# Kernel optimization log

Measured on AMD Instinct MI355X. Metric: run time of the kernel, lower is better.

## Reference

```python
import jax, jax.numpy as jnp
import numpy as np

N = 50000   # nodes
E = 1600000 # edges (avg degree 32)
IN, D, OUT = 128, 256, 128
NUM_MID = 8  # num_layers - 2


def gcn_conv(x, W, b, src, dst, n):
    """PyG GCNConv: add self-loops, symmetric norm, linear transform, scatter-sum."""
    h = x @ W                                           # [n, d_out]
    ones = jnp.ones(src.shape[0], h.dtype)
    deg = jax.ops.segment_sum(ones, dst, num_segments=n) + 1.0  # +1 self-loop
    dinv = jax.lax.rsqrt(deg)                           # deg^{-1/2}
    coef = dinv[src] * dinv[dst]                        # [E]
    agg = jax.ops.segment_sum(h[src] * coef[:, None], dst, num_segments=n)
    agg = agg + h * (dinv * dinv)[:, None]              # self-loop term: dinv[i]^2
    return agg + b


def layer_norm(x, g, b, eps=1e-5):
    mu = jnp.mean(x, axis=-1, keepdims=True)
    var = jnp.mean(jnp.square(x - mu), axis=-1, keepdims=True)
    return (x - mu) * jax.lax.rsqrt(var + eps) * g + b


def setup_inputs() -> dict:
    key = jax.random.key(0)
    ks = jax.random.split(key, 8)
    x = jax.random.normal(ks[0], (N, IN), dtype=jnp.float32)
    edge_index = jax.random.randint(ks[1], (2, E), 0, N, dtype=jnp.int64)
    s_in = 1.0 / np.sqrt(IN)
    s_d = 1.0 / np.sqrt(D)
    return {
        "x": x,
        "edge_index": edge_index,
        "W_in": jax.random.normal(ks[2], (IN, D), dtype=jnp.float32) * s_in,
        "b_in": jnp.zeros((D,), jnp.float32),
        "W_mid": jax.random.normal(ks[3], (NUM_MID, D, D), dtype=jnp.float32) * s_d,
        "b_mid": jnp.zeros((NUM_MID, D), jnp.float32),
        "W_out": jax.random.normal(ks[4], (D, OUT), dtype=jnp.float32) * s_d,
        "b_out": jnp.zeros((OUT,), jnp.float32),
        "gamma": jnp.ones((NUM_MID + 1, D), jnp.float32),
        "beta": jnp.zeros((NUM_MID + 1, D), jnp.float32),
    }


def reference(x, edge_index, W_in, b_in, W_mid, b_mid, W_out, b_out, gamma, beta):
    # Inference mode: dropout is identity.
    src, dst = edge_index[0], edge_index[1]
    n = x.shape[0]
    h = gcn_conv(x, W_in, b_in, src, dst, n)
    h = jax.nn.silu(layer_norm(h, gamma[0], beta[0]))
    for i in range(NUM_MID):  # fixed small layer count
        h = gcn_conv(h, W_mid[i], b_mid[i], src, dst, n)
        h = jax.nn.silu(layer_norm(h, gamma[i + 1], beta[i + 1]))
    return gcn_conv(h, W_out, b_out, src, dst, n)
```

## Files before the change

kernel.cpp:

```cpp
#include <hip/hip_runtime.h>
#include <stdint.h>

#define NN   50000
#define NE   1600000
#define DIN  128
#define DMID 256
#define DOUT 128
#define NMID 8

#define AS1 __attribute__((address_space(1)))
#define AS3 __attribute__((address_space(3)))

typedef unsigned short u16;
typedef unsigned int   u32;
typedef __attribute__((ext_vector_type(8))) short short8;
typedef __attribute__((ext_vector_type(4))) float f32x4;
typedef __attribute__((ext_vector_type(2))) float f32x2;
typedef __attribute__((ext_vector_type(4))) int i32x4;

__device__ __forceinline__ float bf2f(u32 u) {
    union { u32 i; float f; } c; c.i = u << 16; return c.f;
}
__device__ __forceinline__ u16 f2bf(float f) {
    union { float f; u32 i; } c; c.f = f;
    u32 u = c.i;
    return (u16)((u + 0x7fffu + ((u >> 16) & 1u)) >> 16);
}
__device__ __forceinline__ void split2(float v, u16& hi, u16& lo) {
    hi = f2bf(v);
    float r = v - bf2f(hi);
    lo = f2bf(r);
}

__global__ void rank_kernel(const int* __restrict__ ei, int* __restrict__ counts,
                            int* __restrict__ rank) {
    int i = (blockIdx.x * blockDim.x + threadIdx.x) * 4;
    if (i < NE) {
        i32x4 d = *(const i32x4*)(ei + NE + i);
        i32x4 r;
        r.x = atomicAdd(&counts[d.x], 1);
        r.y = atomicAdd(&counts[d.y], 1);
        r.z = atomicAdd(&counts[d.z], 1);
        r.w = atomicAdd(&counts[d.w], 1);
        *(i32x4*)(rank + i) = r;
    }
}

__global__ void dinv_kernel(const int* __restrict__ counts, float* __restrict__ dinv) {
    int i = blockIdx.x * blockDim.x + threadIdx.x;
    if (i < NN) dinv[i] = rsqrtf((float)counts[i] + 1.0f);
}

__global__ __launch_bounds__(1024) void scan_kernel(const int* __restrict__ counts,
                                                    int* __restrict__ rowp) {
    __shared__ int sh[1024];
    const int t = threadIdx.x;
    constexpr int ITEMS = (NN + 1023) / 1024;
    const int start = t * ITEMS;
    int sum = 0;
    for (int j = 0; j < ITEMS; ++j) {
        int idx = start + j;
        if (idx < NN) sum += counts[idx];
    }
    sh[t] = sum;
    __syncthreads();
    for (int offs = 1; offs < 1024; offs <<= 1) {
        int v = (t >= offs) ? sh[t - offs] : 0;
        __syncthreads();
        sh[t] += v;
        __syncthreads();
    }
    int base = (t == 0) ? 0 : sh[t - 1];
    for (int j = 0; j < ITEMS; ++j) {
        int idx = start + j;
        if (idx < NN) {
            rowp[idx] = base;
            base += counts[idx];
        }
    }
    if (t == 0) rowp[NN] = NE;
}

__global__ void scatter_kernel(const int* __restrict__ ei, const int* __restrict__ rowp,
                               const int* __restrict__ rank, int* __restrict__ srcs) {
    int i = (blockIdx.x * blockDim.x + threadIdx.x) * 4;
    if (i < NE) {
        i32x4 d = *(const i32x4*)(ei + NE + i);
        i32x4 s = *(const i32x4*)(ei + i);
        i32x4 r = *(const i32x4*)(rank + i);
        srcs[rowp[d.x] + r.x] = s.x;
        srcs[rowp[d.y] + r.y] = s.y;
        srcs[rowp[d.z] + r.z] = s.z;
        srcs[rowp[d.w] + r.w] = s.w;
    }
}

__global__ void wsplit_kernel(const float* __restrict__ W, u16* __restrict__ Whi,
                              u16* __restrict__ Wlo, int K, int Dc) {
    int idx = blockIdx.x * blockDim.x + threadIdx.x;
    if (idx < K * Dc) {
        int k = idx / Dc, d = idx - k * Dc;
        u16 hi, lo;
        split2(W[idx], hi, lo);
        size_t o = ((size_t)(k >> 5) * Dc + d) * 32 + (k & 31);
        Whi[o] = hi;
        Wlo[o] = lo;
    }
}

__global__ void xsplit_kernel(const float* __restrict__ x, u16* __restrict__ xhi,
                              u16* __restrict__ xlo) {
    int i = blockIdx.x * blockDim.x + threadIdx.x;
    int stride = gridDim.x * blockDim.x;
    for (; i < NN * DIN; i += stride) {
        u16 hi, lo;
        split2(x[i], hi, lo);
        xhi[i] = hi;
        xlo[i] = lo;
    }
}


template <int K, int Dc>
__global__ __launch_bounds__(512, 4) void gemm_kernel(const u16* __restrict__ xhi,
                                                      const u16* __restrict__ xlo,
                                                      const u16* __restrict__ whi,
                                                      const u16* __restrict__ wlo,
                                                      const float* __restrict__ dinv,
                                                      u16* __restrict__ g) {
    constexpr int NTW = Dc / 32;
    constexpr int KS = K / 32;
    __shared__ u16 bh[Dc * 32];
    __shared__ u16 bl[Dc * 32];
    const int tid = threadIdx.x;
    const int wid = tid >> 6;
    const int rowPanel = wid >> 1;
    const int colPanel = wid & 1;
    const int lane = tid & 63;
    const int m = lane & 15, quad = lane >> 4;
    const int rowBase = blockIdx.x * 128 + rowPanel * 32;

    f32x4 acc[2][NTW];
#pragma unroll
    for (int rg = 0; rg < 2; ++rg)
#pragma unroll
        for (int t = 0; t < NTW; ++t) acc[rg][t] = (f32x4){0.f, 0.f, 0.f, 0.f};

    size_t arow[2];
#pragma unroll
    for (int rg = 0; rg < 2; ++rg) {
        int rowA = rowBase + rg * 16 + m;
        if (rowA > NN - 1) rowA = NN - 1;
        arow[rg] = (size_t)rowA * K + quad * 8;
    }

    for (int ks = 0; ks < KS; ++ks) {
        const u16* sh_src = whi + (size_t)ks * Dc * 32;
        const u16* sl_src = wlo + (size_t)ks * Dc * 32;
        __syncthreads();
#pragma unroll
        for (int i = 0; i < Dc * 4; i += 512) {
            int j = i + tid;
            __builtin_amdgcn_global_load_lds((const AS1 void*)(sh_src + j * 8),
                                             (AS3 void*)((AS3 u16*)bh + j * 8), 16, 0, 0);
            __builtin_amdgcn_global_load_lds((const AS1 void*)(sl_src + j * 8),
                                             (AS3 void*)((AS3 u16*)bl + j * 8), 16, 0, 0);
        }
        short8 ah[2], al[2];
#pragma unroll
        for (int rg = 0; rg < 2; ++rg) {
            ah[rg] = *(const short8*)(xhi + arow[rg] + ks * 32);
            al[rg] = *(const short8*)(xlo + arow[rg] + ks * 32);
        }
        __syncthreads();
#pragma unroll
        for (int t = 0; t < NTW; ++t) {
            const int bo = ((colPanel * NTW + t) * 16 + m) * 32 + quad * 8;
            short8 wh = *(const short8*)(bh + bo);
            short8 wl = *(const short8*)(bl + bo);
#pragma unroll
            for (int rg = 0; rg < 2; ++rg) {
                acc[rg][t] = __builtin_amdgcn_mfma_f32_16x16x32_bf16(ah[rg], wh, acc[rg][t], 0, 0, 0);
                acc[rg][t] = __builtin_amdgcn_mfma_f32_16x16x32_bf16(al[rg], wh, acc[rg][t], 0, 0, 0);
                acc[rg][t] = __builtin_amdgcn_mfma_f32_16x16x32_bf16(ah[rg], wl, acc[rg][t], 0, 0, 0);
            }
        }
    }

#pragma unroll
    for (int rg = 0; rg < 2; ++rg) {
        const int r0 = rowBase + rg * 16 + quad * 4;
        float dv[4];
#pragma unroll
        for (int r = 0; r < 4; ++r) {
            int rr = r0 + r;
            dv[r] = (rr < NN) ? dinv[rr] : 0.f;
        }
#pragma unroll
        for (int t = 0; t < NTW; ++t) {
            const int col = colPanel * (Dc / 2) + t * 16 + m;
#pragma unroll
            for (int r = 0; r < 4; ++r) {
                int rr = r0 + r;
                if (rr < NN) g[(size_t)rr * Dc + col] = f2bf(acc[rg][t][r] * dv[r]);
            }
        }
    }
}


template <int L>
__device__ __forceinline__ void loadg(const u16* p, float (&f)[L]);
template <>
__device__ __forceinline__ void loadg<4>(const u16* p, float (&f)[4]) {
    uint2 v = *(const uint2*)p;
    f[0] = bf2f(v.x & 0xffffu); f[1] = bf2f(v.x >> 16);
    f[2] = bf2f(v.y & 0xffffu); f[3] = bf2f(v.y >> 16);
}
template <>
__device__ __forceinline__ void loadg<2>(const u16* p, float (&f)[2]) {
    u32 v = *(const u32*)p;
    f[0] = bf2f(v & 0xffffu); f[1] = bf2f(v >> 16);
}

template <int Dc, bool FINAL>
__global__ __launch_bounds__(256) void agg_kernel(const u16* __restrict__ g,
                                                  const int* __restrict__ rowp,
                                                  const int* __restrict__ srcs,
                                                  const float* __restrict__ dinv,
                                                  const float* __restrict__ bias,
                                                  const float* __restrict__ gamma,
                                                  const float* __restrict__ beta,
                                                  float* __restrict__ outf,
                                                  u16* __restrict__ xhi,
                                                  u16* __restrict__ xlo) {
    constexpr int L = Dc / 64;
    const int wid = threadIdx.x >> 6, lane = threadIdx.x & 63;
    const int node = blockIdx.x * 4 + wid;
    const int coff = lane * L;

    float acc[L];
    loadg<L>(g + (size_t)node * Dc + coff, acc);

    int e = rowp[node];
    const int end = rowp[node + 1];
    for (; e + 8 <= end; e += 8) {
        int s0 = srcs[e],     s1 = srcs[e + 1], s2 = srcs[e + 2], s3 = srcs[e + 3];
        int s4 = srcs[e + 4], s5 = srcs[e + 5], s6 = srcs[e + 6], s7 = srcs[e + 7];
        float f0[L], f1[L], f2[L], f3[L], f4[L], f5[L], f6[L], f7[L];
        loadg<L>(g + (size_t)s0 * Dc + coff, f0);
        loadg<L>(g + (size_t)s1 * Dc + coff, f1);
        loadg<L>(g + (size_t)s2 * Dc + coff, f2);
        loadg<L>(g + (size_t)s3 * Dc + coff, f3);
        loadg<L>(g + (size_t)s4 * Dc + coff, f4);
        loadg<L>(g + (size_t)s5 * Dc + coff, f5);
        loadg<L>(g + (size_t)s6 * Dc + coff, f6);
        loadg<L>(g + (size_t)s7 * Dc + coff, f7);
#pragma unroll
        for (int j = 0; j < L; ++j)
            acc[j] += ((f0[j] + f1[j]) + (f2[j] + f3[j])) +
                      ((f4[j] + f5[j]) + (f6[j] + f7[j]));
    }
    for (; e < end; ++e) {
        float f[L];
        loadg<L>(g + (size_t)srcs[e] * Dc + coff, f);
#pragma unroll
        for (int j = 0; j < L; ++j) acc[j] += f[j];
    }

    const float dv = dinv[node];
    float v[L];
#pragma unroll
    for (int j = 0; j < L; ++j) v[j] = acc[j] * dv + bias[coff + j];

    if (FINAL) {
        if (L == 4) {
            f32x4 o = {v[0], v[1], v[2], v[3]};
            *(f32x4*)(outf + (size_t)node * Dc + coff) = o;
        } else {
            f32x2 o = {v[0], v[1]};
            *(f32x2*)(outf + (size_t)node * Dc + coff) = o;
        }
    } else {
        float s = 0.f, s2 = 0.f;
#pragma unroll
        for (int j = 0; j < L; ++j) {
            s += v[j];
            s2 += v[j] * v[j];
        }
        for (int off = 32; off > 0; off >>= 1) {
            s += __shfl_xor(s, off, 64);
            s2 += __shfl_xor(s2, off, 64);
        }
        const float mu = s * (1.f / Dc);
        const float var = s2 * (1.f / Dc) - mu * mu;
        const float rstd = rsqrtf(fmaxf(var, 0.f) + 1e-5f);
#pragma unroll
        for (int j = 0; j < L; ++j) {
            float y = (v[j] - mu) * rstd * gamma[coff + j] + beta[coff + j];
            v[j] = y / (1.f + __expf(-y));
        }
        u16 hh[L], ll[L];
#pragma unroll
        for (int j = 0; j < L; ++j) split2(v[j], hh[j], ll[j]);
        if (L == 4) {
            uint2 oh, ol;
            oh.x = (u32)hh[0] | ((u32)hh[1] << 16);
            oh.y = (u32)hh[2] | ((u32)hh[3] << 16);
            ol.x = (u32)ll[0] | ((u32)ll[1] << 16);
            ol.y = (u32)ll[2] | ((u32)ll[3] << 16);
            *(uint2*)(xhi + (size_t)node * Dc + coff) = oh;
            *(uint2*)(xlo + (size_t)node * Dc + coff) = ol;
        } else {
            *(u32*)(xhi + (size_t)node * Dc + coff) = (u32)hh[0] | ((u32)hh[1] << 16);
            *(u32*)(xlo + (size_t)node * Dc + coff) = (u32)ll[0] | ((u32)ll[1] << 16);
        }
    }
}


extern "C" void kernel_launch(void* const* d_in, const int* in_sizes, int n_in,
                              void* d_out, int out_size, void* d_ws, size_t ws_size,
                              hipStream_t stream) {
    (void)in_sizes; (void)n_in; (void)out_size; (void)ws_size;
    const float* x_in  = (const float*)d_in[0];
    const int*   ei    = (const int*)d_in[1];
    const float* W_in  = (const float*)d_in[2];
    const float* b_in  = (const float*)d_in[3];
    const float* W_mid = (const float*)d_in[4];
    const float* b_mid = (const float*)d_in[5];
    const float* W_out = (const float*)d_in[6];
    const float* b_out = (const float*)d_in[7];
    const float* gamma = (const float*)d_in[8];
    const float* beta  = (const float*)d_in[9];

    char* ws = (char*)d_ws;
    size_t off = 0;
    auto alloc = [&](size_t bytes) -> char* {
        char* p = ws + off;
        off += (bytes + 255) & ~(size_t)255;
        return p;
    };
    float* dinv   = (float*)alloc((size_t)NN * 4);
    int* counts   = (int*)alloc((size_t)NN * 4);
    int* rowp     = (int*)alloc((size_t)(NN + 1) * 4);
    int* rank     = (int*)alloc((size_t)NE * 4);
    int* srcs     = (int*)alloc((size_t)NE * 4);
    u16* whi_in   = (u16*)alloc((size_t)DIN * DMID * 2);
    u16* wlo_in   = (u16*)alloc((size_t)DIN * DMID * 2);
    u16* whi_mid  = (u16*)alloc((size_t)NMID * DMID * DMID * 2);
    u16* wlo_mid  = (u16*)alloc((size_t)NMID * DMID * DMID * 2);
    u16* whi_out  = (u16*)alloc((size_t)DMID * DOUT * 2);
    u16* wlo_out  = (u16*)alloc((size_t)DMID * DOUT * 2);
    u16* xhi      = (u16*)alloc((size_t)NN * DMID * 2);
    u16* xlo      = (u16*)alloc((size_t)NN * DMID * 2);
    u16* g        = (u16*)alloc((size_t)NN * DMID * 2);

    hipMemsetAsync(counts, 0, (size_t)NN * 4, stream);
    const int EB4 = (NE / 4 + 255) / 256;
    rank_kernel<<<EB4, 256, 0, stream>>>(ei, counts, rank);
    dinv_kernel<<<(NN + 255) / 256, 256, 0, stream>>>(counts, dinv);
    scan_kernel<<<1, 1024, 0, stream>>>(counts, rowp);
    scatter_kernel<<<EB4, 256, 0, stream>>>(ei, rowp, rank, srcs);

    wsplit_kernel<<<(DIN * DMID + 255) / 256, 256, 0, stream>>>(W_in, whi_in, wlo_in, DIN, DMID);
    for (int i = 0; i < NMID; ++i)
        wsplit_kernel<<<(DMID * DMID + 255) / 256, 256, 0, stream>>>(
            W_mid + (size_t)i * DMID * DMID, whi_mid + (size_t)i * DMID * DMID,
            wlo_mid + (size_t)i * DMID * DMID, DMID, DMID);
    wsplit_kernel<<<(DMID * DOUT + 255) / 256, 256, 0, stream>>>(W_out, whi_out, wlo_out, DMID, DOUT);
    xsplit_kernel<<<1024, 256, 0, stream>>>(x_in, xhi, xlo);

    const int GB = (NN + 127) / 128;
    const int NB = NN / 4;

    gemm_kernel<DIN, DMID><<<GB, 512, 0, stream>>>(xhi, xlo, whi_in, wlo_in, dinv, g);
    agg_kernel<DMID, false><<<NB, 256, 0, stream>>>(g, rowp, srcs, dinv, b_in,
                                                    gamma, beta, nullptr, xhi, xlo);
    for (int i = 0; i < NMID; ++i) {
        gemm_kernel<DMID, DMID><<<GB, 512, 0, stream>>>(xhi, xlo,
                                                        whi_mid + (size_t)i * DMID * DMID,
                                                        wlo_mid + (size_t)i * DMID * DMID,
                                                        dinv, g);
        agg_kernel<DMID, false><<<NB, 256, 0, stream>>>(g, rowp, srcs, dinv,
                                                        b_mid + (size_t)i * DMID,
                                                        gamma + (size_t)(i + 1) * DMID,
                                                        beta + (size_t)(i + 1) * DMID,
                                                        nullptr, xhi, xlo);
    }
    gemm_kernel<DMID, DOUT><<<GB, 512, 0, stream>>>(xhi, xlo, whi_out, wlo_out, dinv, g);
    agg_kernel<DOUT, true><<<NB, 256, 0, stream>>>(g, rowp, srcs, dinv, b_out,
                                                   nullptr, nullptr, (float*)d_out,
                                                   nullptr, nullptr);
}
```

Baseline: 1.647 ms.

## Bucket CSR neighbors by source chunk, pad rows, and software-pipeline gathers

The CSR build now groups each node's incoming edges by source-id chunk (source >> 11), so gathers from g walk memory in a more local order. Each row is padded to a multiple of 8 with a dummy index that points at a zeroed extra row of g, which removes the tail loop. The aggregation loop is double-buffered so the next eight row gathers are issued before the current eight are summed, and blocks now hold 8 warps instead of 4. In exchange, preprocessing needs extra kernels and buffers (counts2, rowp2, padded srcs), and the padding adds wasted gather work.

```diff
diff --git a/kernel.cpp b/kernel.cpp
--- a/kernel.cpp
+++ b/kernel.cpp
@@ -7,6 +7,9 @@
 #define DMID 256
 #define DOUT 128
 #define NMID 8
+#define CSH  11
+#define CH   25
+#define PADCAP (NE + 7 * NN)
 
 #define AS1 __attribute__((address_space(1)))
 #define AS3 __attribute__((address_space(3)))
@@ -21,6 +24,12 @@
 __device__ __forceinline__ float bf2f(u32 u) {
     union { u32 i; float f; } c; c.i = u << 16; return c.f;
 }
+__device__ __forceinline__ float ubf_lo(u32 v) {
+    union { u32 i; float f; } c; c.i = v << 16; return c.f;
+}
+__device__ __forceinline__ float ubf_hi(u32 v) {
+    union { u32 i; float f; } c; c.i = v & 0xffff0000u; return c.f;
+}
 __device__ __forceinline__ u16 f2bf(float f) {
     union { float f; u32 i; } c; c.f = f;
     u32 u = c.i;
@@ -32,23 +41,30 @@
     lo = f2bf(r);
 }
 
-__global__ void rank_kernel(const int* __restrict__ ei, int* __restrict__ counts,
+__global__ void rank_kernel(const int* __restrict__ ei, int* __restrict__ counts2,
                             int* __restrict__ rank) {
     int i = (blockIdx.x * blockDim.x + threadIdx.x) * 4;
     if (i < NE) {
         i32x4 d = *(const i32x4*)(ei + NE + i);
+        i32x4 s = *(const i32x4*)(ei + i);
         i32x4 r;
-        r.x = atomicAdd(&counts[d.x], 1);
-        r.y = atomicAdd(&counts[d.y], 1);
-        r.z = atomicAdd(&counts[d.z], 1);
-        r.w = atomicAdd(&counts[d.w], 1);
+        r.x = atomicAdd(&counts2[d.x * CH + (s.x >> CSH)], 1);
+        r.y = atomicAdd(&counts2[d.y * CH + (s.y >> CSH)], 1);
+        r.z = atomicAdd(&counts2[d.z * CH + (s.z >> CSH)], 1);
+        r.w = atomicAdd(&counts2[d.w * CH + (s.w >> CSH)], 1);
         *(i32x4*)(rank + i) = r;
     }
 }
 
-__global__ void dinv_kernel(const int* __restrict__ counts, float* __restrict__ dinv) {
+__global__ void sumc_kernel(const int* __restrict__ counts2, int* __restrict__ counts,
+                            float* __restrict__ dinv) {
     int i = blockIdx.x * blockDim.x + threadIdx.x;
-    if (i < NN) dinv[i] = rsqrtf((float)counts[i] + 1.0f);
+    if (i < NN) {
+        int s = 0;
+        for (int c = 0; c < CH; ++c) s += counts2[i * CH + c];
+        dinv[i] = rsqrtf((float)s + 1.0f);
+        counts[i] = (s + 7) & ~7;
+    }
 }
 
 __global__ __launch_bounds__(1024) void scan_kernel(const int* __restrict__ counts,
@@ -76,22 +92,39 @@
         if (idx < NN) {
             rowp[idx] = base;
             base += counts[idx];
-        }
-    }
-    if (t == 0) rowp[NN] = NE;
-}
-
-__global__ void scatter_kernel(const int* __restrict__ ei, const int* __restrict__ rowp,
+            if (idx == NN - 1) rowp[NN] = base;
+        }
+    }
+}
+
+__global__ void rowp2_kernel(const int* __restrict__ counts2, const int* __restrict__ rowp,
+                             int* __restrict__ rowp2) {
+    int i = blockIdx.x * blockDim.x + threadIdx.x;
+    if (i < NN) {
+        int base = rowp[i];
+        for (int c = 0; c < CH; ++c) {
+            rowp2[i * CH + c] = base;
+            base += counts2[i * CH + c];
+        }
+    }
+}
+
+__global__ void fill_kernel(int* __restrict__ srcs) {
+    int i = (blockIdx.x * blockDim.x + threadIdx.x) * 4;
+    if (i < PADCAP) *(i32x4*)(srcs + i) = (i32x4){NN, NN, NN, NN};
+}
+
+__global__ void scatter_kernel(const int* __restrict__ ei, const int* __restrict__ rowp2,
                                const int* __restrict__ rank, int* __restrict__ srcs) {
     int i = (blockIdx.x * blockDim.x + threadIdx.x) * 4;
     if (i < NE) {
         i32x4 d = *(const i32x4*)(ei + NE + i);
         i32x4 s = *(const i32x4*)(ei + i);
         i32x4 r = *(const i32x4*)(rank + i);
-        srcs[rowp[d.x] + r.x] = s.x;
-        srcs[rowp[d.y] + r.y] = s.y;
-        srcs[rowp[d.z] + r.z] = s.z;
-        srcs[rowp[d.w] + r.w] = s.w;
+        srcs[rowp2[d.x * CH + (s.x >> CSH)] + r.x] = s.x;
+        srcs[rowp2[d.y * CH + (s.y >> CSH)] + r.y] = s.y;
+        srcs[rowp2[d.z * CH + (s.z >> CSH)] + r.z] = s.z;
+        srcs[rowp2[d.w * CH + (s.w >> CSH)] + r.w] = s.w;
     }
 }
 
@@ -119,7 +152,6 @@
         xlo[i] = lo;
     }
 }
-
 
 template <int K, int Dc>
 __global__ __launch_bounds__(512, 4) void gemm_kernel(const u16* __restrict__ xhi,
@@ -214,17 +246,47 @@
 template <>
 __device__ __forceinline__ void loadg<4>(const u16* p, float (&f)[4]) {
     uint2 v = *(const uint2*)p;
-    f[0] = bf2f(v.x & 0xffffu); f[1] = bf2f(v.x >> 16);
-    f[2] = bf2f(v.y & 0xffffu); f[3] = bf2f(v.y >> 16);
+    f[0] = ubf_lo(v.x); f[1] = ubf_hi(v.x);
+    f[2] = ubf_lo(v.y); f[3] = ubf_hi(v.y);
 }
 template <>
 __device__ __forceinline__ void loadg<2>(const u16* p, float (&f)[2]) {
     u32 v = *(const u32*)p;
-    f[0] = bf2f(v & 0xffffu); f[1] = bf2f(v >> 16);
+    f[0] = ubf_lo(v); f[1] = ubf_hi(v);
+}
+
+__device__ __forceinline__ void load_srcs(const int* __restrict__ srcs, int eo,
+                                          int (&S)[8]) {
+#pragma unroll
+    for (int k = 0; k < 8; ++k) S[k] = srcs[eo + k];
+}
+
+template <int Dc, int L>
+__device__ __forceinline__ void issue_rows(const u16* __restrict__ g, const int (&S)[8],
+                                           int coff, uint2 (&R)[8]) {
+#pragma unroll
+    for (int k = 0; k < 8; ++k) {
+        const u16* p = g + (size_t)S[k] * Dc + coff;
+        if constexpr (L == 4) R[k] = *(const uint2*)p;
+        else R[k].x = *(const u32*)p;
+    }
+}
+
+template <int L>
+__device__ __forceinline__ void consume(const uint2 (&R)[8], float (&acc)[L]) {
+#pragma unroll
+    for (int k = 0; k < 8; ++k) {
+        acc[0] += ubf_lo(R[k].x);
+        acc[1] += ubf_hi(R[k].x);
+        if constexpr (L == 4) {
+            acc[2] += ubf_lo(R[k].y);
+            acc[3] += ubf_hi(R[k].y);
+        }
+    }
 }
 
 template <int Dc, bool FINAL>
-__global__ __launch_bounds__(256) void agg_kernel(const u16* __restrict__ g,
+__global__ __launch_bounds__(512) void agg_kernel(const u16* __restrict__ g,
                                                   const int* __restrict__ rowp,
                                                   const int* __restrict__ srcs,
                                                   const float* __restrict__ dinv,
@@ -236,36 +298,38 @@
                                                   u16* __restrict__ xlo) {
     constexpr int L = Dc / 64;
     const int wid = threadIdx.x >> 6, lane = threadIdx.x & 63;
-    const int node = blockIdx.x * 4 + wid;
+    const int node = blockIdx.x * 8 + wid;
     const int coff = lane * L;
 
     float acc[L];
     loadg<L>(g + (size_t)node * Dc + coff, acc);
 
-    int e = rowp[node];
-    const int end = rowp[node + 1];
-    for (; e + 8 <= end; e += 8) {
-        int s0 = srcs[e],     s1 = srcs[e + 1], s2 = srcs[e + 2], s3 = srcs[e + 3];
-        int s4 = srcs[e + 4], s5 = srcs[e + 5], s6 = srcs[e + 6], s7 = srcs[e + 7];
-        float f0[L], f1[L], f2[L], f3[L], f4[L], f5[L], f6[L], f7[L];
-        loadg<L>(g + (size_t)s0 * Dc + coff, f0);
-        loadg<L>(g + (size_t)s1 * Dc + coff, f1);
-        loadg<L>(g + (size_t)s2 * Dc + coff, f2);
-        loadg<L>(g + (size_t)s3 * Dc + coff, f3);
-        loadg<L>(g + (size_t)s4 * Dc + coff, f4);
-        loadg<L>(g + (size_t)s5 * Dc + coff, f5);
-        loadg<L>(g + (size_t)s6 * Dc + coff, f6);
-        loadg<L>(g + (size_t)s7 * Dc + coff, f7);
-#pragma unroll
-        for (int j = 0; j < L; ++j)
-            acc[j] += ((f0[j] + f1[j]) + (f2[j] + f3[j])) +
-                      ((f4[j] + f5[j]) + (f6[j] + f7[j]));
-    }
-    for (; e < end; ++e) {
-        float f[L];
-        loadg<L>(g + (size_t)srcs[e] * Dc + coff, f);
-#pragma unroll
-        for (int j = 0; j < L; ++j) acc[j] += f[j];
+    const int e0 = rowp[node];
+    const int nb = (rowp[node + 1] - e0) >> 3;
+
+    if (nb > 0) {
+        const int last = e0 + (nb - 1) * 8;
+        int S[8];
+        uint2 rA[8], rB[8];
+        load_srcs(srcs, e0, S);
+        issue_rows<Dc, L>(g, S, coff, rA);
+        load_srcs(srcs, nb > 1 ? e0 + 8 : e0, S);
+        int b = 0;
+        for (;;) {
+            issue_rows<Dc, L>(g, S, coff, rB);
+            int ec = e0 + (b + 2) * 8;
+            ec = ec > last ? last : ec;
+            load_srcs(srcs, ec, S);
+            consume<L>(rA, acc);
+            if (b + 1 >= nb) break;
+            issue_rows<Dc, L>(g, S, coff, rA);
+            ec = e0 + (b + 3) * 8;
+            ec = ec > last ? last : ec;
+            load_srcs(srcs, ec, S);
+            consume<L>(rB, acc);
+            if (b + 2 >= nb) break;
+            b += 2;
+        }
     }
 
     const float dv = dinv[node];
@@ -344,8 +408,10 @@
     float* dinv   = (float*)alloc((size_t)NN * 4);
     int* counts   = (int*)alloc((size_t)NN * 4);
     int* rowp     = (int*)alloc((size_t)(NN + 1) * 4);
+    int* counts2  = (int*)alloc((size_t)NN * CH * 4);
+    int* rowp2    = (int*)alloc((size_t)NN * CH * 4);
     int* rank     = (int*)alloc((size_t)NE * 4);
-    int* srcs     = (int*)alloc((size_t)NE * 4);
+    int* srcs     = (int*)alloc((size_t)PADCAP * 4);
     u16* whi_in   = (u16*)alloc((size_t)DIN * DMID * 2);
     u16* wlo_in   = (u16*)alloc((size_t)DIN * DMID * 2);
     u16* whi_mid  = (u16*)alloc((size_t)NMID * DMID * DMID * 2);
@@ -354,14 +420,19 @@
     u16* wlo_out  = (u16*)alloc((size_t)DMID * DOUT * 2);
     u16* xhi      = (u16*)alloc((size_t)NN * DMID * 2);
     u16* xlo      = (u16*)alloc((size_t)NN * DMID * 2);
-    u16* g        = (u16*)alloc((size_t)NN * DMID * 2);
-
-    hipMemsetAsync(counts, 0, (size_t)NN * 4, stream);
+    u16* g        = (u16*)alloc(((size_t)NN + 1) * DMID * 2);
+
+    hipMemsetAsync(counts2, 0, (size_t)NN * CH * 4, stream);
+    hipMemsetAsync((char*)g + (size_t)NN * DMID * 2, 0, DMID * 2, stream);
+
     const int EB4 = (NE / 4 + 255) / 256;
-    rank_kernel<<<EB4, 256, 0, stream>>>(ei, counts, rank);
-    dinv_kernel<<<(NN + 255) / 256, 256, 0, stream>>>(counts, dinv);
+    const int NBK = (NN + 255) / 256;
+    rank_kernel<<<EB4, 256, 0, stream>>>(ei, counts2, rank);
+    sumc_kernel<<<NBK, 256, 0, stream>>>(counts2, counts, dinv);
     scan_kernel<<<1, 1024, 0, stream>>>(counts, rowp);
-    scatter_kernel<<<EB4, 256, 0, stream>>>(ei, rowp, rank, srcs);
+    rowp2_kernel<<<NBK, 256, 0, stream>>>(counts2, rowp, rowp2);
+    fill_kernel<<<(PADCAP / 4 + 255) / 256, 256, 0, stream>>>(srcs);
+    scatter_kernel<<<EB4, 256, 0, stream>>>(ei, rowp2, rank, srcs);
 
     wsplit_kernel<<<(DIN * DMID + 255) / 256, 256, 0, stream>>>(W_in, whi_in, wlo_in, DIN, DMID);
     for (int i = 0; i < NMID; ++i)
@@ -372,24 +443,25 @@
     xsplit_kernel<<<1024, 256, 0, stream>>>(x_in, xhi, xlo);
 
     const int GB = (NN + 127) / 128;
-    const int NB = NN / 4;
+    const int AB = NN / 8;
 
     gemm_kernel<DIN, DMID><<<GB, 512, 0, stream>>>(xhi, xlo, whi_in, wlo_in, dinv, g);
-    agg_kernel<DMID, false><<<NB, 256, 0, stream>>>(g, rowp, srcs, dinv, b_in,
+    agg_kernel<DMID, false><<<AB, 512, 0, stream>>>(g, rowp, srcs, dinv, b_in,
                                                     gamma, beta, nullptr, xhi, xlo);
     for (int i = 0; i < NMID; ++i) {
         gemm_kernel<DMID, DMID><<<GB, 512, 0, stream>>>(xhi, xlo,
                                                         whi_mid + (size_t)i * DMID * DMID,
                                                         wlo_mid + (size_t)i * DMID * DMID,
                                                         dinv, g);
-        agg_kernel<DMID, false><<<NB, 256, 0, stream>>>(g, rowp, srcs, dinv,
+        agg_kernel<DMID, false><<<AB, 512, 0, stream>>>(g, rowp, srcs, dinv,
                                                         b_mid + (size_t)i * DMID,
                                                         gamma + (size_t)(i + 1) * DMID,
                                                         beta + (size_t)(i + 1) * DMID,
                                                         nullptr, xhi, xlo);
     }
     gemm_kernel<DMID, DOUT><<<GB, 512, 0, stream>>>(xhi, xlo, whi_out, wlo_out, dinv, g);
-    agg_kernel<DOUT, true><<<NB, 256, 0, stream>>>(g, rowp, srcs, dinv, b_out,
+    hipMemsetAsync((char*)g + (size_t)NN * DOUT * 2, 0, DOUT * 2, stream);
+    agg_kernel<DOUT, true><<<AB, 512, 0, stream>>>(g, rowp, srcs, dinv, b_out,
                                                    nullptr, nullptr, (float*)d_out,
                                                    nullptr, nullptr);
 }
```

Result: no change. 1.668 ms (+1.3%).

## Slice feature matrix into 32-column panels, pad CSR to 8, use 16-bit source indices

Applied to the files above, without the earlier changes.

The GEMM now writes its output in column-sliced panels of 32 features, so each aggregation block gathers one small slice and its working set is more likely to stay in cache. The CSR is padded to multiples of 8 with a zeroed sentinel row and stored as 16-bit indices, which halves index traffic and removes the tail loop. LayerNorm is split into a separate kernel that combines per-slice partial sums. In exchange, an fp32 intermediate and an extra launch per layer add memory traffic, and the 16-bit indices rely on the node count fitting in 16 bits.

```diff
diff --git a/kernel.cpp b/kernel.cpp
--- a/kernel.cpp
+++ b/kernel.cpp
@@ -7,6 +7,7 @@
 #define DMID 256
 #define DOUT 128
 #define NMID 8
+#define PADCAP (NE + 7 * NN)
 
 #define AS1 __attribute__((address_space(1)))
 #define AS3 __attribute__((address_space(3)))
@@ -20,6 +21,12 @@
 
 __device__ __forceinline__ float bf2f(u32 u) {
     union { u32 i; float f; } c; c.i = u << 16; return c.f;
+}
+__device__ __forceinline__ float ubf_lo(u32 v) {
+    union { u32 i; float f; } c; c.i = v << 16; return c.f;
+}
+__device__ __forceinline__ float ubf_hi(u32 v) {
+    union { u32 i; float f; } c; c.i = v & 0xffff0000u; return c.f;
 }
 __device__ __forceinline__ u16 f2bf(float f) {
     union { float f; u32 i; } c; c.f = f;
@@ -46,12 +53,17 @@
     }
 }
 
-__global__ void dinv_kernel(const int* __restrict__ counts, float* __restrict__ dinv) {
+__global__ void pad_kernel(const int* __restrict__ counts, int* __restrict__ cpad,
+                           float* __restrict__ dinv) {
     int i = blockIdx.x * blockDim.x + threadIdx.x;
-    if (i < NN) dinv[i] = rsqrtf((float)counts[i] + 1.0f);
-}
-
-__global__ __launch_bounds__(1024) void scan_kernel(const int* __restrict__ counts,
+    if (i < NN) {
+        int c = counts[i];
+        dinv[i] = rsqrtf((float)c + 1.0f);
+        cpad[i] = (c + 7) & ~7;
+    }
+}
+
+__global__ __launch_bounds__(1024) void scan_kernel(const int* __restrict__ cpad,
                                                     int* __restrict__ rowp) {
     __shared__ int sh[1024];
     const int t = threadIdx.x;
@@ -60,7 +72,7 @@
     int sum = 0;
     for (int j = 0; j < ITEMS; ++j) {
         int idx = start + j;
-        if (idx < NN) sum += counts[idx];
+        if (idx < NN) sum += cpad[idx];
     }
     sh[t] = sum;
     __syncthreads();
@@ -75,24 +87,37 @@
         int idx = start + j;
         if (idx < NN) {
             rowp[idx] = base;
-            base += counts[idx];
-        }
-    }
-    if (t == 0) rowp[NN] = NE;
-}
-
-__global__ void scatter_kernel(const int* __restrict__ ei, const int* __restrict__ rowp,
-                               const int* __restrict__ rank, int* __restrict__ srcs) {
+            base += cpad[idx];
+            if (idx == NN - 1) rowp[NN] = base;
+        }
+    }
+}
+
+__global__ void fill16_kernel(u16* __restrict__ srcs) {
+    int i = (blockIdx.x * blockDim.x + threadIdx.x) * 8;
+    if (i < PADCAP) {
+        const int v = NN | (NN << 16);
+        *(i32x4*)(srcs + i) = (i32x4){v, v, v, v};
+    }
+}
+
+__global__ void scatter16_kernel(const int* __restrict__ ei, const int* __restrict__ rowp,
+                                 const int* __restrict__ rank, u16* __restrict__ srcs) {
     int i = (blockIdx.x * blockDim.x + threadIdx.x) * 4;
     if (i < NE) {
         i32x4 d = *(const i32x4*)(ei + NE + i);
         i32x4 s = *(const i32x4*)(ei + i);
         i32x4 r = *(const i32x4*)(rank + i);
-        srcs[rowp[d.x] + r.x] = s.x;
-        srcs[rowp[d.y] + r.y] = s.y;
-        srcs[rowp[d.z] + r.z] = s.z;
-        srcs[rowp[d.w] + r.w] = s.w;
-    }
+        srcs[rowp[d.x] + r.x] = (u16)s.x;
+        srcs[rowp[d.y] + r.y] = (u16)s.y;
+        srcs[rowp[d.z] + r.z] = (u16)s.z;
+        srcs[rowp[d.w] + r.w] = (u16)s.w;
+    }
+}
+
+__global__ void zsent_kernel(u16* __restrict__ gs) {
+    int s = threadIdx.x >> 5, c = threadIdx.x & 31;
+    gs[((size_t)s * (NN + 1) + NN) * 32 + c] = 0;
 }
 
 __global__ void wsplit_kernel(const float* __restrict__ W, u16* __restrict__ Whi,
@@ -120,14 +145,13 @@
     }
 }
 
-
 template <int K, int Dc>
 __global__ __launch_bounds__(512, 4) void gemm_kernel(const u16* __restrict__ xhi,
                                                       const u16* __restrict__ xlo,
                                                       const u16* __restrict__ whi,
                                                       const u16* __restrict__ wlo,
                                                       const float* __restrict__ dinv,
-                                                      u16* __restrict__ g) {
+                                                      u16* __restrict__ gs) {
     constexpr int NTW = Dc / 32;
     constexpr int KS = K / 32;
     __shared__ u16 bh[Dc * 32];
@@ -202,120 +226,139 @@
 #pragma unroll
             for (int r = 0; r < 4; ++r) {
                 int rr = r0 + r;
-                if (rr < NN) g[(size_t)rr * Dc + col] = f2bf(acc[rg][t][r] * dv[r]);
+                if (rr < NN) {
+                    size_t o = ((size_t)(col >> 5) * (NN + 1) + rr) * 32 + (col & 31);
+                    gs[o] = f2bf(acc[rg][t][r] * dv[r]);
+                }
             }
         }
     }
 }
 
 
-template <int L>
-__device__ __forceinline__ void loadg(const u16* p, float (&f)[L]);
-template <>
-__device__ __forceinline__ void loadg<4>(const u16* p, float (&f)[4]) {
-    uint2 v = *(const uint2*)p;
-    f[0] = bf2f(v.x & 0xffffu); f[1] = bf2f(v.x >> 16);
-    f[2] = bf2f(v.y & 0xffffu); f[3] = bf2f(v.y >> 16);
-}
-template <>
-__device__ __forceinline__ void loadg<2>(const u16* p, float (&f)[2]) {
-    u32 v = *(const u32*)p;
-    f[0] = bf2f(v & 0xffffu); f[1] = bf2f(v >> 16);
+__device__ __forceinline__ void loadS(const u16* __restrict__ srcs, int eo, int (&S)[8]) {
+    i32x4 v = *(const i32x4*)(srcs + eo);
+    S[0] = v.x & 0xffff; S[1] = (v.x >> 16) & 0xffff;
+    S[2] = v.y & 0xffff; S[3] = (v.y >> 16) & 0xffff;
+    S[4] = v.z & 0xffff; S[5] = (v.z >> 16) & 0xffff;
+    S[6] = v.w & 0xffff; S[7] = (v.w >> 16) & 0xffff;
 }
 
 template <int Dc, bool FINAL>
-__global__ __launch_bounds__(256) void agg_kernel(const u16* __restrict__ g,
+__global__ __launch_bounds__(256) void agg_kernel(const u16* __restrict__ gs,
                                                   const int* __restrict__ rowp,
-                                                  const int* __restrict__ srcs,
+                                                  const u16* __restrict__ srcs,
                                                   const float* __restrict__ dinv,
                                                   const float* __restrict__ bias,
-                                                  const float* __restrict__ gamma,
-                                                  const float* __restrict__ beta,
-                                                  float* __restrict__ outf,
-                                                  u16* __restrict__ xhi,
-                                                  u16* __restrict__ xlo) {
-    constexpr int L = Dc / 64;
+                                                  float* __restrict__ vs,
+                                                  float* __restrict__ part,
+                                                  float* __restrict__ outf) {
+    constexpr int NSL = Dc / 32;
+    constexpr int SH = (NSL == 8) ? 3 : 2;
+    const int slice = blockIdx.x & (NSL - 1);
+    const int grp = blockIdx.x >> SH;
+    const int wid = threadIdx.x >> 6, lane = threadIdx.x & 63;
+    const int node = grp * 4 + wid;
+    const int eg = lane >> 4, cs = lane & 15;
+
+    const u32* gsl = (const u32*)gs + (size_t)slice * (NN + 1) * 16 + cs;
+
+    float a0, a1;
+    {
+        u32 v = gsl[node * 16];
+        a0 = (eg == 0) ? ubf_lo(v) : 0.f;
+        a1 = (eg == 0) ? ubf_hi(v) : 0.f;
+    }
+
+    const int e0 = rowp[node];
+    const int nb = (rowp[node + 1] - e0) >> 3;
+
+    if (nb > 0) {
+        const int last = e0 + (nb - 1) * 8;
+        int S[8];
+        u32 A0, A1, B0, B1;
+        loadS(srcs, e0, S);
+        A0 = gsl[S[eg] * 16]; A1 = gsl[S[eg + 4] * 16];
+        loadS(srcs, nb > 1 ? e0 + 8 : e0, S);
+        int b = 0;
+        for (;;) {
+            B0 = gsl[S[eg] * 16]; B1 = gsl[S[eg + 4] * 16];
+            int ec = e0 + (b + 2) * 8;
+            ec = ec > last ? last : ec;
+            loadS(srcs, ec, S);
+            a0 += ubf_lo(A0) + ubf_lo(A1);
+            a1 += ubf_hi(A0) + ubf_hi(A1);
+            if (b + 1 >= nb) break;
+            A0 = gsl[S[eg] * 16]; A1 = gsl[S[eg + 4] * 16];
+            ec = e0 + (b + 3) * 8;
+            ec = ec > last ? last : ec;
+            loadS(srcs, ec, S);
+            a0 += ubf_lo(B0) + ubf_lo(B1);
+            a1 += ubf_hi(B0) + ubf_hi(B1);
+            if (b + 2 >= nb) break;
+            b += 2;
+        }
+    }
+
+    a0 += __shfl_xor(a0, 16, 64); a0 += __shfl_xor(a0, 32, 64);
+    a1 += __shfl_xor(a1, 16, 64); a1 += __shfl_xor(a1, 32, 64);
+
+    const float dv = dinv[node];
+    const int f = slice * 32 + cs * 2;
+    const float v0 = a0 * dv + bias[f];
+    const float v1 = a1 * dv + bias[f + 1];
+
+    if (FINAL) {
+        if (eg == 0) *(f32x2*)(outf + (size_t)node * Dc + f) = (f32x2){v0, v1};
+    } else {
+        if (eg == 0)
+            *(f32x2*)(vs + ((size_t)slice * NN + node) * 32 + cs * 2) = (f32x2){v0, v1};
+        float p1 = v0 + v1, p2 = v0 * v0 + v1 * v1;
+        p1 += __shfl_xor(p1, 1, 64); p2 += __shfl_xor(p2, 1, 64);
+        p1 += __shfl_xor(p1, 2, 64); p2 += __shfl_xor(p2, 2, 64);
+        p1 += __shfl_xor(p1, 4, 64); p2 += __shfl_xor(p2, 4, 64);
+        p1 += __shfl_xor(p1, 8, 64); p2 += __shfl_xor(p2, 8, 64);
+        if (lane == 0)
+            *(f32x2*)(part + ((size_t)node * NSL + slice) * 2) = (f32x2){p1, p2};
+    }
+}
+
+__global__ __launch_bounds__(256) void ln_kernel(const float* __restrict__ vs,
+                                                 const float* __restrict__ part,
+                                                 const float* __restrict__ gamma,
+                                                 const float* __restrict__ beta,
+                                                 u16* __restrict__ xhi,
+                                                 u16* __restrict__ xlo) {
     const int wid = threadIdx.x >> 6, lane = threadIdx.x & 63;
     const int node = blockIdx.x * 4 + wid;
-    const int coff = lane * L;
-
-    float acc[L];
-    loadg<L>(g + (size_t)node * Dc + coff, acc);
-
-    int e = rowp[node];
-    const int end = rowp[node + 1];
-    for (; e + 8 <= end; e += 8) {
-        int s0 = srcs[e],     s1 = srcs[e + 1], s2 = srcs[e + 2], s3 = srcs[e + 3];
-        int s4 = srcs[e + 4], s5 = srcs[e + 5], s6 = srcs[e + 6], s7 = srcs[e + 7];
-        float f0[L], f1[L], f2[L], f3[L], f4[L], f5[L], f6[L], f7[L];
-        loadg<L>(g + (size_t)s0 * Dc + coff, f0);
-        loadg<L>(g + (size_t)s1 * Dc + coff, f1);
-        loadg<L>(g + (size_t)s2 * Dc + coff, f2);
-        loadg<L>(g + (size_t)s3 * Dc + coff, f3);
-        loadg<L>(g + (size_t)s4 * Dc + coff, f4);
-        loadg<L>(g + (size_t)s5 * Dc + coff, f5);
-        loadg<L>(g + (size_t)s6 * Dc + coff, f6);
-        loadg<L>(g + (size_t)s7 * Dc + coff, f7);
-#pragma unroll
-        for (int j = 0; j < L; ++j)
-            acc[j] += ((f0[j] + f1[j]) + (f2[j] + f3[j])) +
-                      ((f4[j] + f5[j]) + (f6[j] + f7[j]));
-    }
-    for (; e < end; ++e) {
-        float f[L];
-        loadg<L>(g + (size_t)srcs[e] * Dc + coff, f);
-#pragma unroll
-        for (int j = 0; j < L; ++j) acc[j] += f[j];
-    }
-
-    const float dv = dinv[node];
-    float v[L];
-#pragma unroll
-    for (int j = 0; j < L; ++j) v[j] = acc[j] * dv + bias[coff + j];
-
-    if (FINAL) {
-        if (L == 4) {
-            f32x4 o = {v[0], v[1], v[2], v[3]};
-            *(f32x4*)(outf + (size_t)node * Dc + coff) = o;
-        } else {
-            f32x2 o = {v[0], v[1]};
-            *(f32x2*)(outf + (size_t)node * Dc + coff) = o;
-        }
-    } else {
-        float s = 0.f, s2 = 0.f;
-#pragma unroll
-        for (int j = 0; j < L; ++j) {
-            s += v[j];
-            s2 += v[j] * v[j];
-        }
-        for (int off = 32; off > 0; off >>= 1) {
-            s += __shfl_xor(s, off, 64);
-            s2 += __shfl_xor(s2, off, 64);
-        }
-        const float mu = s * (1.f / Dc);
-        const float var = s2 * (1.f / Dc) - mu * mu;
-        const float rstd = rsqrtf(fmaxf(var, 0.f) + 1e-5f);
-#pragma unroll
-        for (int j = 0; j < L; ++j) {
-            float y = (v[j] - mu) * rstd * gamma[coff + j] + beta[coff + j];
-            v[j] = y / (1.f + __expf(-y));
-        }
-        u16 hh[L], ll[L];
-#pragma unroll
-        for (int j = 0; j < L; ++j) split2(v[j], hh[j], ll[j]);
-        if (L == 4) {
-            uint2 oh, ol;
-            oh.x = (u32)hh[0] | ((u32)hh[1] << 16);
-            oh.y = (u32)hh[2] | ((u32)hh[3] << 16);
-            ol.x = (u32)ll[0] | ((u32)ll[1] << 16);
-            ol.y = (u32)ll[2] | ((u32)ll[3] << 16);
-            *(uint2*)(xhi + (size_t)node * Dc + coff) = oh;
-            *(uint2*)(xlo + (size_t)node * Dc + coff) = ol;
-        } else {
-            *(u32*)(xhi + (size_t)node * Dc + coff) = (u32)hh[0] | ((u32)hh[1] << 16);
-            *(u32*)(xlo + (size_t)node * Dc + coff) = (u32)ll[0] | ((u32)ll[1] << 16);
-        }
-    }
+    const int s = lane >> 3, o = (lane & 7) * 4;
+
+    f32x4 vv = *(const f32x4*)(vs + ((size_t)s * NN + node) * 32 + o);
+    f32x2 p = *(const f32x2*)(part + ((size_t)node * 8 + (lane & 7)) * 2);
+    float s1 = p.x, s2 = p.y;
+    s1 += __shfl_xor(s1, 1, 64); s2 += __shfl_xor(s2, 1, 64);
+    s1 += __shfl_xor(s1, 2, 64); s2 += __shfl_xor(s2, 2, 64);
+    s1 += __shfl_xor(s1, 4, 64); s2 += __shfl_xor(s2, 4, 64);
+
+    const float mu = s1 * (1.f / 256.f);
+    const float var = s2 * (1.f / 256.f) - mu * mu;
+    const float rstd = rsqrtf(fmaxf(var, 0.f) + 1e-5f);
+
+    const int f = s * 32 + o;
+    u16 hh[4], ll[4];
+#pragma unroll
+    for (int j = 0; j < 4; ++j) {
+        float y = (vv[j] - mu) * rstd * gamma[f + j] + beta[f + j];
+        y = y / (1.f + __expf(-y));
+        split2(y, hh[j], ll[j]);
+    }
+    uint2 oh, ol;
+    oh.x = (u32)hh[0] | ((u32)hh[1] << 16);
+    oh.y = (u32)hh[2] | ((u32)hh[3] << 16);
+    ol.x = (u32)ll[0] | ((u32)ll[1] << 16);
+    ol.y = (u32)ll[2] | ((u32)ll[3] << 16);
+    *(uint2*)(xhi + (size_t)node * 256 + f) = oh;
+    *(uint2*)(xlo + (size_t)node * 256 + f) = ol;
 }
 
 
@@ -343,9 +386,10 @@
     };
     float* dinv   = (float*)alloc((size_t)NN * 4);
     int* counts   = (int*)alloc((size_t)NN * 4);
+    int* cpad     = (int*)alloc((size_t)NN * 4);
     int* rowp     = (int*)alloc((size_t)(NN + 1) * 4);
     int* rank     = (int*)alloc((size_t)NE * 4);
-    int* srcs     = (int*)alloc((size_t)NE * 4);
+    u16* srcs     = (u16*)alloc((size_t)PADCAP * 2);
     u16* whi_in   = (u16*)alloc((size_t)DIN * DMID * 2);
     u16* wlo_in   = (u16*)alloc((size_t)DIN * DMID * 2);
     u16* whi_mid  = (u16*)alloc((size_t)NMID * DMID * DMID * 2);
@@ -354,14 +398,20 @@
     u16* wlo_out  = (u16*)alloc((size_t)DMID * DOUT * 2);
     u16* xhi      = (u16*)alloc((size_t)NN * DMID * 2);
     u16* xlo      = (u16*)alloc((size_t)NN * DMID * 2);
-    u16* g        = (u16*)alloc((size_t)NN * DMID * 2);
+    u16* gs       = (u16*)alloc((size_t)8 * (NN + 1) * 32 * 2);
+    float* vs     = (float*)alloc((size_t)NN * DMID * 4);
+    float* part   = (float*)alloc((size_t)NN * 8 * 2 * 4);
 
     hipMemsetAsync(counts, 0, (size_t)NN * 4, stream);
+
     const int EB4 = (NE / 4 + 255) / 256;
+    const int NBK = (NN + 255) / 256;
     rank_kernel<<<EB4, 256, 0, stream>>>(ei, counts, rank);
-    dinv_kernel<<<(NN + 255) / 256, 256, 0, stream>>>(counts, dinv);
-    scan_kernel<<<1, 1024, 0, stream>>>(counts, rowp);
-    scatter_kernel<<<EB4, 256, 0, stream>>>(ei, rowp, rank, srcs);
+    pad_kernel<<<NBK, 256, 0, stream>>>(counts, cpad, dinv);
+    scan_kernel<<<1, 1024, 0, stream>>>(cpad, rowp);
+    fill16_kernel<<<(PADCAP / 8 + 255) / 256, 256, 0, stream>>>(srcs);
+    scatter16_kernel<<<EB4, 256, 0, stream>>>(ei, rowp, rank, srcs);
+    zsent_kernel<<<1, 256, 0, stream>>>(gs);
 
     wsplit_kernel<<<(DIN * DMID + 255) / 256, 256, 0, stream>>>(W_in, whi_in, wlo_in, DIN, DMID);
     for (int i = 0; i < NMID; ++i)
@@ -372,24 +422,27 @@
     xsplit_kernel<<<1024, 256, 0, stream>>>(x_in, xhi, xlo);
 
     const int GB = (NN + 127) / 128;
-    const int NB = NN / 4;
-
-    gemm_kernel<DIN, DMID><<<GB, 512, 0, stream>>>(xhi, xlo, whi_in, wlo_in, dinv, g);
-    agg_kernel<DMID, false><<<NB, 256, 0, stream>>>(g, rowp, srcs, dinv, b_in,
-                                                    gamma, beta, nullptr, xhi, xlo);
+    const int AGM = (NN / 4) * 8;
+    const int AGF = (NN / 4) * 4;
+    const int LNB = NN / 4;
+
+    gemm_kernel<DIN, DMID><<<GB, 512, 0, stream>>>(xhi, xlo, whi_in, wlo_in, dinv, gs);
+    agg_kernel<DMID, false><<<AGM, 256, 0, stream>>>(gs, rowp, srcs, dinv, b_in,
+                                                     vs, part, nullptr);
+    ln_kernel<<<LNB, 256, 0, stream>>>(vs, part, gamma, beta, xhi, xlo);
     for (int i = 0; i < NMID; ++i) {
         gemm_kernel<DMID, DMID><<<GB, 512, 0, stream>>>(xhi, xlo,
                                                         whi_mid + (size_t)i * DMID * DMID,
                                                         wlo_mid + (size_t)i * DMID * DMID,
-                                                        dinv, g);
-        agg_kernel<DMID, false><<<NB, 256, 0, stream>>>(g, rowp, srcs, dinv,
-                                                        b_mid + (size_t)i * DMID,
-                                                        gamma + (size_t)(i + 1) * DMID,
-                                                        beta + (size_t)(i + 1) * DMID,
-                                                        nullptr, xhi, xlo);
-    }
-    gemm_kernel<DMID, DOUT><<<GB, 512, 0, stream>>>(xhi, xlo, whi_out, wlo_out, dinv, g);
-    agg_kernel<DOUT, true><<<NB, 256, 0, stream>>>(g, rowp, srcs, dinv, b_out,
-                                                   nullptr, nullptr, (float*)d_out,
-                                                   nullptr, nullptr);
-}
+                                                        dinv, gs);
+        agg_kernel<DMID, false><<<AGM, 256, 0, stream>>>(gs, rowp, srcs, dinv,
+                                                         b_mid + (size_t)i * DMID,
+                                                         vs, part, nullptr);
+        ln_kernel<<<LNB, 256, 0, stream>>>(vs, part,
+                                           gamma + (size_t)(i + 1) * DMID,
+                                           beta + (size_t)(i + 1) * DMID, xhi, xlo);
+    }
+    gemm_kernel<DMID, DOUT><<<GB, 512, 0, stream>>>(xhi, xlo, whi_out, wlo_out, dinv, gs);
+    agg_kernel<DOUT, true><<<AGF, 256, 0, stream>>>(gs, rowp, srcs, dinv, b_out,
+                                                    nullptr, nullptr, (float*)d_out);
+}
```

New measurement: 2.744 ms. 66.5% more time.
